# Optimization experiments

Measured on AMD Instinct MI355X. Metric: run time of the kernel, lower is better.

Reference implementation:

```python
import jax, jax.numpy as jnp
import numpy as np

SEG_NUM = 100000
D_SEG = 128
D_S = 258       # 2*D_SEG + 2 (offset)
D_M7 = 512
D_M8 = 256
MASK = 64
T_SLOTS = 96
B = 4096
CAND_OUT = 4            # candidate_layer out_features
DW_COLS = D_M8 - CAND_OUT  # 252
BN_EPS = 1e-6
COS_EPS = 1e-8


def setup_inputs() -> dict:
    key = jax.random.key(0)
    ks = jax.random.split(key, 20)
    s = 0.02
    return {
        "src": jax.random.randint(ks[0], (B,), 0, SEG_NUM),
        "dest": jax.random.randint(ks[1], (B,), 0, SEG_NUM),
        "t": jax.random.randint(ks[2], (B,), 0, T_SLOTS),
        "candidates": jax.random.randint(ks[3], (B, MASK), 0, SEG_NUM),
        "offset": jax.random.normal(ks[4], (B, 4), jnp.float32),
        "emb_feat": jax.random.normal(ks[5], (SEG_NUM, D_SEG), jnp.float32) * s,
        "emb_dest": jax.random.normal(ks[6], (SEG_NUM, D_SEG), jnp.float32) * s,
        "w1": jax.random.normal(ks[7], (D_M7, D_S), jnp.float32) * s,
        "b1": jnp.zeros((D_M7,), jnp.float32),
        "bn_gamma": jnp.ones((D_M7,), jnp.float32),
        "bn_beta": jnp.zeros((D_M7,), jnp.float32),
        "bn_mean": jax.random.normal(ks[8], (D_M7,), jnp.float32) * s,
        "bn_var": jax.random.uniform(ks[9], (D_M7,), jnp.float32, 0.5, 1.5),
        "w2": jax.random.normal(ks[10], (D_M8, D_M7), jnp.float32) * s,
        "b2": jnp.zeros((D_M8,), jnp.float32),
        "dense_w": jax.random.normal(ks[11], (SEG_NUM, DW_COLS), jnp.float32) * s,
        "dense_b": jnp.zeros((SEG_NUM,), jnp.float32),
        "cand_w": jax.random.normal(ks[12], (CAND_OUT, 2), jnp.float32) * s,
        "cand_b": jnp.zeros((CAND_OUT,), jnp.float32),
        "segs_src": jax.random.normal(ks[13], (SEG_NUM, 2), jnp.float32),
        "segs_trg": jax.random.normal(ks[14], (SEG_NUM, 2), jnp.float32),
        "traffic_pop": jax.random.uniform(ks[15], (SEG_NUM, T_SLOTS), jnp.float32),
    }


def reference(src, dest, t, candidates, offset, emb_feat, emb_dest, w1, b1,
              bn_gamma, bn_beta, bn_mean, bn_var, w2, b2, dense_w, dense_b,
              cand_w, cand_b, segs_src, segs_trg, traffic_pop):
    # --- ODEncoder: embedding gathers + offset features ---
    code = jnp.concatenate([emb_feat[src], emb_dest[dest], offset[:, 1:3]], axis=1)  # [B, 258]
    # --- MLP: Linear -> BatchNorm1d (eval, running stats) -> ReLU -> Linear ---
    h = code @ w1.T + b1
    h = (h - bn_mean) * (bn_gamma / jnp.sqrt(bn_var + BN_EPS)) + bn_beta
    h = jax.nn.relu(h)
    out = h @ w2.T + b2  # [B, 256]
    # --- gather dense rows by candidate index ---
    sub_w = dense_w[candidates]   # [B, M, 252]
    sub_b = dense_b[candidates]   # [B, M]
    # --- traffic feature: traffic_pop[candidate, t] ---
    traffic_feat = traffic_pop[candidates, t[:, None]]  # [B, M]
    # --- cosine similarity between dest-direction and segment direction ---
    v1 = segs_src[dest][:, None, :] - segs_src[candidates]  # [B, M, 2]
    v2 = segs_trg[candidates] - segs_src[candidates]        # [B, M, 2]
    num = jnp.sum(v1 * v2, axis=-1)
    den = jnp.maximum(jnp.linalg.norm(v1, axis=-1) * jnp.linalg.norm(v2, axis=-1), COS_EPS)
    cos_feat = num / den  # [B, M]
    cand_feat = jnp.stack([cos_feat, traffic_feat], axis=-1)  # [B, M, 2]
    emb_cand = cand_feat @ cand_w.T + cand_b                  # [B, M, 4]
    W = jnp.concatenate([sub_w, emb_cand], axis=-1)           # [B, M, 256]
    # --- batched small matvec + bias ---
    logits = jnp.einsum('bmd,bd->bm', W, out) + sub_b         # [B, M]
    return logits
```

## Files before the change

kernel.cpp:

```cpp
#include <hip/hip_runtime.h>


#define BATCH 4096
#define DSEG 128
#define DS_ 258
#define DM7 512
#define DM8 256
#define NCAND 64
#define DWC 252
#define TSLOTS 96
#define SEGN 100000

typedef short bf16x8 __attribute__((ext_vector_type(8)));
typedef short bf16x4 __attribute__((ext_vector_type(4)));
typedef float f32x4 __attribute__((ext_vector_type(4)));

static __device__ __forceinline__ short f2bf(float f) {
    union { float f; unsigned u; } v; v.f = f;
    unsigned r = (v.u + 0x7FFFu + ((v.u >> 16) & 1u)) >> 16;
    return (short)r;
}
static __device__ __forceinline__ float bfu2f(unsigned u16hi) {
    union { unsigned u; float f; } v; v.u = u16hi << 16; return v.f;
}

__global__ __launch_bounds__(512) void mlp_conv_kernel(
    const int* __restrict__ src, const int* __restrict__ dest,
    const float* __restrict__ offset,
    const float* __restrict__ emb_feat, const float* __restrict__ emb_dest,
    const float* __restrict__ w1, const float* __restrict__ b1,
    const float* __restrict__ bn_gamma, const float* __restrict__ bn_beta,
    const float* __restrict__ bn_mean, const float* __restrict__ bn_var,
    const float* __restrict__ w2, const float* __restrict__ b2,
    const float* __restrict__ dense_w, short* __restrict__ wtab,
    float* __restrict__ out_ws)
{
    const int tid = threadIdx.x;

    if (blockIdx.x >= BATCH / 16) {
        const size_t nthr = (size_t)(gridDim.x - BATCH / 16) * 512;
        const size_t g0 = (size_t)(blockIdx.x - BATCH / 16) * 512 + tid;
        const float4* __restrict__ src4 = (const float4*)dense_w;
        bf16x4* __restrict__ dst4 = (bf16x4*)wtab;
        const size_t n4 = (size_t)SEGN * DWC / 4;
        for (size_t i = g0; i < n4; i += nthr) {
            const float4 v = src4[i];
            bf16x4 s;
            s[0] = f2bf(v.x); s[1] = f2bf(v.y); s[2] = f2bf(v.z); s[3] = f2bf(v.w);
            dst4[i] = s;
        }
        return;
    }

    __shared__ __align__(16) short hlds[16][520];
    const int w    = tid >> 6;
    const int lane = tid & 63;
    const int lg   = lane >> 4;
    const int lr   = lane & 15;
    const int b0   = blockIdx.x * 16;

    const int si = src[b0 + lr];
    const int di = dest[b0 + lr];
    const float* fb = emb_feat + (size_t)si * DSEG;
    const float* db = emb_dest + (size_t)di * DSEG;
    bf16x8 a1[8];
#pragma unroll
    for (int s = 0; s < 8; ++s) {
        const float* p = (s < 4) ? (fb + s * 32 + lg * 8)
                                 : (db + (s - 4) * 32 + lg * 8);
        const float4 x = *(const float4*)p;
        const float4 y = *(const float4*)(p + 4);
        bf16x8 t;
        t[0] = f2bf(x.x); t[1] = f2bf(x.y); t[2] = f2bf(x.z); t[3] = f2bf(x.w);
        t[4] = f2bf(y.x); t[5] = f2bf(y.y); t[6] = f2bf(y.z); t[7] = f2bf(y.w);
        a1[s] = t;
    }
    float off1[4], off2[4];
#pragma unroll
    for (int q = 0; q < 4; ++q) {
        const float4 o = *(const float4*)(offset + (size_t)(b0 + lg * 4 + q) * 4);
        off1[q] = o.y; off2[q] = o.z;
    }

#pragma unroll
    for (int nt = 0; nt < 4; ++nt) {
        const int n = (w * 4 + nt) * 16 + lr;
        const float* wrow = w1 + (size_t)n * DS_;
        f32x4 acc = {0.f, 0.f, 0.f, 0.f};
#pragma unroll
        for (int s = 0; s < 8; ++s) {
            const float* p = wrow + s * 32 + lg * 8;
            const float2 x0 = *(const float2*)(p);
            const float2 x1 = *(const float2*)(p + 2);
            const float2 x2 = *(const float2*)(p + 4);
            const float2 x3 = *(const float2*)(p + 6);
            bf16x8 bb;
            bb[0] = f2bf(x0.x); bb[1] = f2bf(x0.y); bb[2] = f2bf(x1.x); bb[3] = f2bf(x1.y);
            bb[4] = f2bf(x2.x); bb[5] = f2bf(x2.y); bb[6] = f2bf(x3.x); bb[7] = f2bf(x3.y);
            acc = __builtin_amdgcn_mfma_f32_16x16x32_bf16(a1[s], bb, acc, 0, 0, 0);
        }
        const float2 wtail = *(const float2*)(wrow + 256);
        const float scale = bn_gamma[n] / sqrtf(bn_var[n] + 1e-6f);
        const float shift = bn_beta[n] - bn_mean[n] * scale;
        const float bias  = b1[n];
#pragma unroll
        for (int q = 0; q < 4; ++q) {
            float v = acc[q] + bias + off1[q] * wtail.x + off2[q] * wtail.y;
            v = fmaf(v, scale, shift);
            v = fmaxf(v, 0.f);
            hlds[lg * 4 + q][n] = f2bf(v);
        }
    }
    __syncthreads();

    bf16x8 a2[16];
#pragma unroll
    for (int s = 0; s < 16; ++s) {
        a2[s] = *(const bf16x8*)&hlds[lr][s * 32 + lg * 8];
    }
#pragma unroll
    for (int nt = 0; nt < 2; ++nt) {
        const int n = (w * 2 + nt) * 16 + lr;
        const float* wrow = w2 + (size_t)n * DM7;
        f32x4 acc = {0.f, 0.f, 0.f, 0.f};
#pragma unroll
        for (int s = 0; s < 16; ++s) {
            const float4 x = *(const float4*)(wrow + s * 32 + lg * 8);
            const float4 y = *(const float4*)(wrow + s * 32 + lg * 8 + 4);
            bf16x8 bb;
            bb[0] = f2bf(x.x); bb[1] = f2bf(x.y); bb[2] = f2bf(x.z); bb[3] = f2bf(x.w);
            bb[4] = f2bf(y.x); bb[5] = f2bf(y.y); bb[6] = f2bf(y.z); bb[7] = f2bf(y.w);
            acc = __builtin_amdgcn_mfma_f32_16x16x32_bf16(a2[s], bb, acc, 0, 0, 0);
        }
        const float bias = b2[n];
#pragma unroll
        for (int q = 0; q < 4; ++q) {
            out_ws[(size_t)(b0 + lg * 4 + q) * DM8 + n] = acc[q] + bias;
        }
    }
}

template <bool BF16TAB>
__global__ __launch_bounds__(256) void logits_kernel_t(
    const int* __restrict__ dest, const int* __restrict__ tt,
    const int* __restrict__ candidates,
    const float* __restrict__ dense_w, const unsigned short* __restrict__ wtab,
    const float* __restrict__ dense_b,
    const float* __restrict__ cand_w, const float* __restrict__ cand_b,
    const float* __restrict__ segs_src, const float* __restrict__ segs_trg,
    const float* __restrict__ traffic_pop,
    const float* __restrict__ out_ws,
    float* __restrict__ logits)
{
    __shared__ float plds[4][16][67];
    const int b = blockIdx.x;
    const int tid = threadIdx.x;
    const int wave = tid >> 6;
    const int lane = tid & 63;
    const int mbase = wave * 16;

    int candv = 0;
    if (lane < 16) candv = candidates[b * NCAND + mbase + lane];

    const int ll = (lane < 63) ? lane : 62;
    float4 dwf[16];
    uint2  dwb[16];
    if (BF16TAB) {
#pragma unroll
        for (int i = 0; i < 16; ++i) {
            const int ci = __shfl(candv, i, 64);
            dwb[i] = *(const uint2*)(wtab + (size_t)ci * DWC + ll * 4);
        }
    } else {
#pragma unroll
        for (int i = 0; i < 16; ++i) {
            const int ci = __shfl(candv, i, 64);
            dwf[i] = *(const float4*)(dense_w + (size_t)ci * DWC + ll * 4);
        }
    }

    float4 o4 = *(const float4*)(out_ws + (size_t)b * DM8 + ll * 4);
    if (lane == 63) { o4.x = 0.f; o4.y = 0.f; o4.z = 0.f; o4.w = 0.f; }

    float tail = 0.f;
    if (lane < 16) {
        const float4 t4 = *(const float4*)(out_ws + (size_t)b * DM8 + DWC);
        const int db = dest[b];
        const float2 dsx = *(const float2*)(segs_src + 2 * (size_t)db);
        const float2 sx = *(const float2*)(segs_src + 2 * (size_t)candv);
        const float2 tx = *(const float2*)(segs_trg + 2 * (size_t)candv);
        const float v1x = dsx.x - sx.x, v1y = dsx.y - sx.y;
        const float v2x = tx.x - sx.x, v2y = tx.y - sx.y;
        const float num = v1x * v2x + v1y * v2y;
        const float den = fmaxf(sqrtf(v1x * v1x + v1y * v1y) *
                                sqrtf(v2x * v2x + v2y * v2y), 1e-8f);
        const float cosv = num / den;
        const float tf = traffic_pop[(size_t)candv * TSLOTS + tt[b]];
        const float e0 = fmaf(cosv, cand_w[0], fmaf(tf, cand_w[1], cand_b[0]));
        const float e1 = fmaf(cosv, cand_w[2], fmaf(tf, cand_w[3], cand_b[1]));
        const float e2 = fmaf(cosv, cand_w[4], fmaf(tf, cand_w[5], cand_b[2]));
        const float e3 = fmaf(cosv, cand_w[6], fmaf(tf, cand_w[7], cand_b[3]));
        tail = e0 * t4.x + e1 * t4.y + e2 * t4.z + e3 * t4.w + dense_b[candv];
    }

#pragma unroll
    for (int i = 0; i < 16; ++i) {
        float p;
        if (BF16TAB) {
            p =        bfu2f(dwb[i].x & 0xFFFFu)  * o4.x;
            p = fmaf(  bfu2f(dwb[i].x >> 16),       o4.y, p);
            p = fmaf(  bfu2f(dwb[i].y & 0xFFFFu),   o4.z, p);
            p = fmaf(  bfu2f(dwb[i].y >> 16),       o4.w, p);
        } else {
            p = dwf[i].x * o4.x + dwf[i].y * o4.y + dwf[i].z * o4.z + dwf[i].w * o4.w;
        }
        plds[wave][i][lane] = p;
    }
    __syncthreads();

    const int cc = lane >> 2;
    const int qq = lane & 3;
    float s = 0.f;
#pragma unroll
    for (int j = 0; j < 16; ++j) s += plds[wave][cc][qq * 16 + j];
    s += __shfl_xor(s, 1, 64);
    s += __shfl_xor(s, 2, 64);
    const float tl = __shfl(tail, cc, 64);
    if (qq == 0) logits[(size_t)b * NCAND + mbase + cc] = s + tl;
}

extern "C" void kernel_launch(void* const* d_in, const int* in_sizes, int n_in,
                              void* d_out, int out_size, void* d_ws, size_t ws_size,
                              hipStream_t stream) {
    const int*   src         = (const int*)d_in[0];
    const int*   dest        = (const int*)d_in[1];
    const int*   tt          = (const int*)d_in[2];
    const int*   candidates  = (const int*)d_in[3];
    const float* offset      = (const float*)d_in[4];
    const float* emb_feat    = (const float*)d_in[5];
    const float* emb_dest    = (const float*)d_in[6];
    const float* w1          = (const float*)d_in[7];
    const float* b1          = (const float*)d_in[8];
    const float* bn_gamma    = (const float*)d_in[9];
    const float* bn_beta     = (const float*)d_in[10];
    const float* bn_mean     = (const float*)d_in[11];
    const float* bn_var      = (const float*)d_in[12];
    const float* w2          = (const float*)d_in[13];
    const float* b2          = (const float*)d_in[14];
    const float* dense_w     = (const float*)d_in[15];
    const float* dense_b     = (const float*)d_in[16];
    const float* cand_w      = (const float*)d_in[17];
    const float* cand_b      = (const float*)d_in[18];
    const float* segs_src    = (const float*)d_in[19];
    const float* segs_trg    = (const float*)d_in[20];
    const float* traffic_pop = (const float*)d_in[21];

    float* out_ws = (float*)d_ws;
    const size_t OUT_WS_BYTES = (size_t)BATCH * DM8 * 4;
    const size_t WTAB_BYTES = (size_t)SEGN * DWC * 2;
    short* wtab = (short*)((char*)d_ws + OUT_WS_BYTES);
    const bool use_bf16 = ws_size >= OUT_WS_BYTES + WTAB_BYTES;
    float* logits = (float*)d_out;

    const int nblk = use_bf16 ? (BATCH / 16) * 2 : (BATCH / 16);
    mlp_conv_kernel<<<nblk, 512, 0, stream>>>(
        src, dest, offset, emb_feat, emb_dest,
        w1, b1, bn_gamma, bn_beta, bn_mean, bn_var, w2, b2,
        dense_w, wtab, out_ws);

    if (use_bf16) {
        logits_kernel_t<true><<<BATCH, 256, 0, stream>>>(
            dest, tt, candidates, dense_w, (const unsigned short*)wtab, dense_b,
            cand_w, cand_b, segs_src, segs_trg, traffic_pop, out_ws, logits);
    } else {
        logits_kernel_t<false><<<BATCH, 256, 0, stream>>>(
            dest, tt, candidates, dense_w, (const unsigned short*)wtab, dense_b,
            cand_w, cand_b, segs_src, segs_trg, traffic_pop, out_ws, logits);
    }
}
```

Measured before the change: 86.39 us.

## Split weight conversion into a separate kernel and pre-convert MLP weights to bf16

Conversion of dense_w, w1 and w2 to bf16 now runs in its own kernel. The dense_w loop is unrolled four ways. The MLP kernel then loads pre-converted bf16 weight tiles instead of converting fp32 weights in every block, which removes redundant per-block conversion and halves weight load bytes. The cost is an extra kernel launch and serialization: the MLP no longer overlaps with the dense_w conversion, and it needs extra workspace.

Result: faster. 83.03 us (-3.9%).

```diff
diff --git a/kernel.cpp b/kernel.cpp
--- a/kernel.cpp
+++ b/kernel.cpp
@@ -10,6 +10,8 @@
 #define DWC 252
 #define TSLOTS 96
 #define SEGN 100000
+#define CONV_BLOCKS 2048
+#define CONV_DW_BLOCKS 2016
 
 typedef short bf16x8 __attribute__((ext_vector_type(8)));
 typedef short bf16x4 __attribute__((ext_vector_type(4)));
@@ -20,11 +22,54 @@
     unsigned r = (v.u + 0x7FFFu + ((v.u >> 16) & 1u)) >> 16;
     return (short)r;
 }
-static __device__ __forceinline__ float bfu2f(unsigned u16hi) {
-    union { unsigned u; float f; } v; v.u = u16hi << 16; return v.f;
-}
-
-__global__ __launch_bounds__(512) void mlp_conv_kernel(
+static __device__ __forceinline__ bf16x4 cvt4(float4 v) {
+    bf16x4 s;
+    s[0] = f2bf(v.x); s[1] = f2bf(v.y); s[2] = f2bf(v.z); s[3] = f2bf(v.w);
+    return s;
+}
+static __device__ __forceinline__ float bfu2f(unsigned u16) {
+    union { unsigned u; float f; } v; v.u = u16 << 16; return v.f;
+}
+
+__global__ __launch_bounds__(256) void conv_kernel(
+    const float* __restrict__ dense_w, const float* __restrict__ w1,
+    const float* __restrict__ w2,
+    short* __restrict__ wtab, short* __restrict__ w1tab, short* __restrict__ w2tab)
+{
+    const int tid = threadIdx.x;
+    if (blockIdx.x < CONV_DW_BLOCKS) {
+        const size_t S = (size_t)CONV_DW_BLOCKS * 256;
+        const size_t n4 = (size_t)SEGN * DWC / 4;
+        size_t i = (size_t)blockIdx.x * 256 + tid;
+        const float4* __restrict__ s4 = (const float4*)dense_w;
+        bf16x4* __restrict__ d4 = (bf16x4*)wtab;
+        for (; i + 3 * S < n4; i += 4 * S) {
+            const float4 v0 = s4[i];
+            const float4 v1 = s4[i + S];
+            const float4 v2 = s4[i + 2 * S];
+            const float4 v3 = s4[i + 3 * S];
+            d4[i]         = cvt4(v0);
+            d4[i + S]     = cvt4(v1);
+            d4[i + 2 * S] = cvt4(v2);
+            d4[i + 3 * S] = cvt4(v3);
+        }
+        for (; i < n4; i += S) d4[i] = cvt4(s4[i]);
+    } else if (blockIdx.x < CONV_DW_BLOCKS + 16) {
+        for (int e = (blockIdx.x - CONV_DW_BLOCKS) * 256 + tid; e < 32768; e += 4096) {
+            const int n = e >> 6, k4 = e & 63;
+            const float4 v = *(const float4*)(w1 + (size_t)n * DS_ + k4 * 4);
+            *(bf16x4*)(w1tab + n * 256 + k4 * 4) = cvt4(v);
+        }
+    } else {
+        for (int e = (blockIdx.x - CONV_DW_BLOCKS - 16) * 256 + tid; e < 32768; e += 4096) {
+            const float4 v = *(const float4*)(w2 + (size_t)e * 4);
+            *(bf16x4*)(w2tab + (size_t)e * 4) = cvt4(v);
+        }
+    }
+}
+
+template <bool TAB>
+__global__ __launch_bounds__(512) void mlp_kernel_t(
     const int* __restrict__ src, const int* __restrict__ dest,
     const float* __restrict__ offset,
     const float* __restrict__ emb_feat, const float* __restrict__ emb_dest,
@@ -32,27 +77,11 @@
     const float* __restrict__ bn_gamma, const float* __restrict__ bn_beta,
     const float* __restrict__ bn_mean, const float* __restrict__ bn_var,
     const float* __restrict__ w2, const float* __restrict__ b2,
-    const float* __restrict__ dense_w, short* __restrict__ wtab,
+    const short* __restrict__ w1tab, const short* __restrict__ w2tab,
     float* __restrict__ out_ws)
 {
+    __shared__ __align__(16) short hlds[16][520];
     const int tid = threadIdx.x;
-
-    if (blockIdx.x >= BATCH / 16) {
-        const size_t nthr = (size_t)(gridDim.x - BATCH / 16) * 512;
-        const size_t g0 = (size_t)(blockIdx.x - BATCH / 16) * 512 + tid;
-        const float4* __restrict__ src4 = (const float4*)dense_w;
-        bf16x4* __restrict__ dst4 = (bf16x4*)wtab;
-        const size_t n4 = (size_t)SEGN * DWC / 4;
-        for (size_t i = g0; i < n4; i += nthr) {
-            const float4 v = src4[i];
-            bf16x4 s;
-            s[0] = f2bf(v.x); s[1] = f2bf(v.y); s[2] = f2bf(v.z); s[3] = f2bf(v.w);
-            dst4[i] = s;
-        }
-        return;
-    }
-
-    __shared__ __align__(16) short hlds[16][520];
     const int w    = tid >> 6;
     const int lane = tid & 63;
     const int lg   = lane >> 4;
@@ -85,21 +114,24 @@
 #pragma unroll
     for (int nt = 0; nt < 4; ++nt) {
         const int n = (w * 4 + nt) * 16 + lr;
-        const float* wrow = w1 + (size_t)n * DS_;
         f32x4 acc = {0.f, 0.f, 0.f, 0.f};
 #pragma unroll
         for (int s = 0; s < 8; ++s) {
-            const float* p = wrow + s * 32 + lg * 8;
-            const float2 x0 = *(const float2*)(p);
-            const float2 x1 = *(const float2*)(p + 2);
-            const float2 x2 = *(const float2*)(p + 4);
-            const float2 x3 = *(const float2*)(p + 6);
             bf16x8 bb;
-            bb[0] = f2bf(x0.x); bb[1] = f2bf(x0.y); bb[2] = f2bf(x1.x); bb[3] = f2bf(x1.y);
-            bb[4] = f2bf(x2.x); bb[5] = f2bf(x2.y); bb[6] = f2bf(x3.x); bb[7] = f2bf(x3.y);
+            if (TAB) {
+                bb = *(const bf16x8*)(w1tab + (size_t)n * 256 + s * 32 + lg * 8);
+            } else {
+                const float* p = w1 + (size_t)n * DS_ + s * 32 + lg * 8;
+                const float2 x0 = *(const float2*)(p);
+                const float2 x1 = *(const float2*)(p + 2);
+                const float2 x2 = *(const float2*)(p + 4);
+                const float2 x3 = *(const float2*)(p + 6);
+                bb[0] = f2bf(x0.x); bb[1] = f2bf(x0.y); bb[2] = f2bf(x1.x); bb[3] = f2bf(x1.y);
+                bb[4] = f2bf(x2.x); bb[5] = f2bf(x2.y); bb[6] = f2bf(x3.x); bb[7] = f2bf(x3.y);
+            }
             acc = __builtin_amdgcn_mfma_f32_16x16x32_bf16(a1[s], bb, acc, 0, 0, 0);
         }
-        const float2 wtail = *(const float2*)(wrow + 256);
+        const float2 wtail = *(const float2*)(w1 + (size_t)n * DS_ + 256);
         const float scale = bn_gamma[n] / sqrtf(bn_var[n] + 1e-6f);
         const float shift = bn_beta[n] - bn_mean[n] * scale;
         const float bias  = b1[n];
@@ -121,15 +153,18 @@
 #pragma unroll
     for (int nt = 0; nt < 2; ++nt) {
         const int n = (w * 2 + nt) * 16 + lr;
-        const float* wrow = w2 + (size_t)n * DM7;
         f32x4 acc = {0.f, 0.f, 0.f, 0.f};
 #pragma unroll
         for (int s = 0; s < 16; ++s) {
-            const float4 x = *(const float4*)(wrow + s * 32 + lg * 8);
-            const float4 y = *(const float4*)(wrow + s * 32 + lg * 8 + 4);
             bf16x8 bb;
-            bb[0] = f2bf(x.x); bb[1] = f2bf(x.y); bb[2] = f2bf(x.z); bb[3] = f2bf(x.w);
-            bb[4] = f2bf(y.x); bb[5] = f2bf(y.y); bb[6] = f2bf(y.z); bb[7] = f2bf(y.w);
+            if (TAB) {
+                bb = *(const bf16x8*)(w2tab + (size_t)n * 512 + s * 32 + lg * 8);
+            } else {
+                const float4 x = *(const float4*)(w2 + (size_t)n * DM7 + s * 32 + lg * 8);
+                const float4 y = *(const float4*)(w2 + (size_t)n * DM7 + s * 32 + lg * 8 + 4);
+                bb[0] = f2bf(x.x); bb[1] = f2bf(x.y); bb[2] = f2bf(x.z); bb[3] = f2bf(x.w);
+                bb[4] = f2bf(y.x); bb[5] = f2bf(y.y); bb[6] = f2bf(y.z); bb[7] = f2bf(y.w);
+            }
             acc = __builtin_amdgcn_mfma_f32_16x16x32_bf16(a2[s], bb, acc, 0, 0, 0);
         }
         const float bias = b2[n];
@@ -207,10 +242,10 @@
     for (int i = 0; i < 16; ++i) {
         float p;
         if (BF16TAB) {
-            p =        bfu2f(dwb[i].x & 0xFFFFu)  * o4.x;
-            p = fmaf(  bfu2f(dwb[i].x >> 16),       o4.y, p);
-            p = fmaf(  bfu2f(dwb[i].y & 0xFFFFu),   o4.z, p);
-            p = fmaf(  bfu2f(dwb[i].y >> 16),       o4.w, p);
+            p =      bfu2f(dwb[i].x & 0xFFFFu) * o4.x;
+            p = fmaf(bfu2f(dwb[i].x >> 16),      o4.y, p);
+            p = fmaf(bfu2f(dwb[i].y & 0xFFFFu),  o4.z, p);
+            p = fmaf(bfu2f(dwb[i].y >> 16),      o4.w, p);
         } else {
             p = dwf[i].x * o4.x + dwf[i].y * o4.y + dwf[i].z * o4.z + dwf[i].w * o4.w;
         }
@@ -257,22 +292,28 @@
 
     float* out_ws = (float*)d_ws;
     const size_t OUT_WS_BYTES = (size_t)BATCH * DM8 * 4;
-    const size_t WTAB_BYTES = (size_t)SEGN * DWC * 2;
-    short* wtab = (short*)((char*)d_ws + OUT_WS_BYTES);
-    const bool use_bf16 = ws_size >= OUT_WS_BYTES + WTAB_BYTES;
+    const size_t WTAB_BYTES   = (size_t)SEGN * DWC * 2;
+    const size_t W1TAB_BYTES  = (size_t)DM7 * 256 * 2;
+    const size_t W2TAB_BYTES  = (size_t)DM8 * DM7 * 2;
+    short* wtab  = (short*)((char*)d_ws + OUT_WS_BYTES);
+    short* w1tab = (short*)((char*)d_ws + OUT_WS_BYTES + WTAB_BYTES);
+    short* w2tab = (short*)((char*)d_ws + OUT_WS_BYTES + WTAB_BYTES + W1TAB_BYTES);
+    const bool use_tab =
+        ws_size >= OUT_WS_BYTES + WTAB_BYTES + W1TAB_BYTES + W2TAB_BYTES;
     float* logits = (float*)d_out;
 
-    const int nblk = use_bf16 ? (BATCH / 16) * 2 : (BATCH / 16);
-    mlp_conv_kernel<<<nblk, 512, 0, stream>>>(
-        src, dest, offset, emb_feat, emb_dest,
-        w1, b1, bn_gamma, bn_beta, bn_mean, bn_var, w2, b2,
-        dense_w, wtab, out_ws);
-
-    if (use_bf16) {
+    if (use_tab) {
+        conv_kernel<<<CONV_BLOCKS, 256, 0, stream>>>(dense_w, w1, w2, wtab, w1tab, w2tab);
+        mlp_kernel_t<true><<<BATCH / 16, 512, 0, stream>>>(
+            src, dest, offset, emb_feat, emb_dest,
+            w1, b1, bn_gamma, bn_beta, bn_mean, bn_var, w2, b2, w1tab, w2tab, out_ws);
         logits_kernel_t<true><<<BATCH, 256, 0, stream>>>(
             dest, tt, candidates, dense_w, (const unsigned short*)wtab, dense_b,
             cand_w, cand_b, segs_src, segs_trg, traffic_pop, out_ws, logits);
     } else {
+        mlp_kernel_t<false><<<BATCH / 16, 512, 0, stream>>>(
+            src, dest, offset, emb_feat, emb_dest,
+            w1, b1, bn_gamma, bn_beta, bn_mean, bn_var, w2, b2, w1tab, w2tab, out_ws);
         logits_kernel_t<false><<<BATCH, 256, 0, stream>>>(
             dest, tt, candidates, dense_w, (const unsigned short*)wtab, dense_b,
             cand_w, cand_b, segs_src, segs_trg, traffic_pop, out_ws, logits);
```
